# Kernel optimization log

Measured on AMD Instinct MI355X. Metric: run time of the kernel, lower is better.

The kernel has to match this reference:

```python
import jax, jax.numpy as jnp
import numpy as np

B, N, D_MODEL, LAP = 64, 64, 256, 16


def setup_inputs() -> dict:
    key = jax.random.key(0)
    ks = jax.random.split(key, 8)
    adj = jax.random.randint(ks[0], (B, N, N), 0, 2, dtype=jnp.int32)
    node_feats = jax.random.normal(ks[1], (B, N, D_MODEL), dtype=jnp.float32)
    eigvec = jax.random.normal(ks[2], (B, N, LAP), dtype=jnp.float32)
    W_lap = jax.random.normal(ks[3], (LAP, D_MODEL), dtype=jnp.float32) / np.sqrt(LAP)
    W_edge = jax.random.normal(ks[4], (1 + 2 * LAP, D_MODEL), dtype=jnp.float32) / np.sqrt(1 + 2 * LAP)
    b_edge = jax.random.normal(ks[5], (D_MODEL,), dtype=jnp.float32) * 0.02
    type_embed = jax.random.normal(ks[6], (2, D_MODEL), dtype=jnp.float32)
    graph_tok = jax.random.normal(ks[7], (1, 1, D_MODEL), dtype=jnp.float32)
    return {"adj": adj, "node_feats": node_feats, "eigvec": eigvec,
            "W_lap": W_lap, "W_edge": W_edge, "b_edge": b_edge,
            "type_embed": type_embed, "graph_tok": graph_tok}


def reference(adj, node_feats, eigvec, W_lap, W_edge, b_edge, type_embed, graph_tok):
    b, n, _ = adj.shape
    d = graph_tok.shape[-1]
    # node tokens: feats + LapPE projection
    node_tok = node_feats + jnp.einsum('bnl,ld->bnd', eigvec, W_lap)
    # upper-triangular candidate edges (fixed M = n(n-1)/2, jit-friendly)
    iu, ju = jnp.triu_indices(n, k=1)               # [M]
    valid = adj[:, iu, ju] > 0                       # [B, M]
    # stable compaction: valid edges first (matches torch per-graph extraction order)
    order = jnp.argsort(~valid, axis=1, stable=True) # [B, M]
    src = iu[order]                                  # [B, M]
    dst = ju[order]
    valid_sorted = jnp.take_along_axis(valid, order, axis=1)
    Pu = jnp.take_along_axis(eigvec, src[..., None], axis=1)  # [B, M, LAP]
    Pv = jnp.take_along_axis(eigvec, dst[..., None], axis=1)
    m = src.shape[1]
    edge_in = jnp.concatenate([jnp.ones((b, m, 1), eigvec.dtype), Pu, Pv], axis=-1)
    etok = jnp.einsum('bmf,fd->bmd', edge_in, W_edge) + b_edge + type_embed[1]
    etok = jnp.where(valid_sorted[..., None], etok, 0.0)      # zeros at padding
    pad_mask_edges = ~valid_sorted                             # True = padding
    gtok = jnp.broadcast_to(graph_tok, (b, 1, d))
    seq_embeds = jnp.concatenate([gtok, node_tok, etok], axis=1)  # [B, 1+n+M, d]
    pad_mask = jnp.concatenate([jnp.zeros((b, 1 + n), bool), pad_mask_edges], axis=1)
    return seq_embeds, pad_mask
```

## Files before the change

kernel.cpp:

```cpp
#include <hip/hip_runtime.h>

#define B_ 64
#define N_ 64
#define D_ 256
#define LAP_ 16
#define M_ 2016
#define TOK_ 2081

__global__ __launch_bounds__(256) void compact_kernel(const int* __restrict__ adj,
                                                      int* __restrict__ pack) {
    int b = blockIdx.x;
    int t = threadIdx.x;
    __shared__ int s[256];
    __shared__ int s_total;

    int ii[8], jj[8], vv[8];
    int c = 0;
#pragma unroll
    for (int k = 0; k < 8; k++) {
        int m = t * 8 + k;
        int valid = 0, i = 0, j = 0;
        if (m < M_) {
            float fm = (float)m;
            int gi = (int)((127.0f - sqrtf(127.0f * 127.0f - 8.0f * fm)) * 0.5f);
            if (gi < 0) gi = 0;
            if (gi > 62) gi = 62;
            while (gi > 0 && (127 * gi - gi * gi) / 2 > m) gi--;
            while (gi < 62 && (127 * (gi + 1) - (gi + 1) * (gi + 1)) / 2 <= m) gi++;
            i = gi;
            j = i + 1 + (m - (127 * i - i * i) / 2);
            valid = (adj[b * (N_ * N_) + i * N_ + j] > 0) ? 1 : 0;
        }
        ii[k] = i; jj[k] = j; vv[k] = valid;
        c += valid;
    }
    s[t] = c;
    __syncthreads();
    for (int off = 1; off < 256; off <<= 1) {
        int v = (t >= off) ? s[t - off] : 0;
        __syncthreads();
        s[t] += v;
        __syncthreads();
    }
    if (t == 255) s_total = s[255];
    __syncthreads();
    int total = s_total;
    int run = s[t] - c;
#pragma unroll
    for (int k = 0; k < 8; k++) {
        int m = t * 8 + k;
        if (m < M_) {
            int p;
            if (vv[k]) { p = run; run++; }
            else       { p = total + (m - run); }
            pack[b * M_ + p] = ii[k] | (jj[k] << 8) | (vv[k] << 16);
        }
    }
}

__global__ __launch_bounds__(256) void node_kernel(const float* __restrict__ node_feats,
                                                   const float* __restrict__ eigvec,
                                                   const float* __restrict__ W_lap,
                                                   const float* __restrict__ graph_tok,
                                                   float* __restrict__ out) {
    int b = blockIdx.x;
    int t = threadIdx.x;
    int n = blockIdx.y * 4 + (t >> 6);
    int lane = t & 63;
    const float* e = eigvec + (size_t)(b * N_ + n) * LAP_;
    float4 acc = ((const float4*)(node_feats + ((size_t)b * N_ + n) * D_))[lane];
#pragma unroll
    for (int l = 0; l < LAP_; l++) {
        float el = e[l];
        float4 w = ((const float4*)(W_lap + l * D_))[lane];
        acc.x += el * w.x; acc.y += el * w.y; acc.z += el * w.z; acc.w += el * w.w;
    }
    ((float4*)(out + (size_t)b * TOK_ * D_ + (size_t)(1 + n) * D_))[lane] = acc;

    if (blockIdx.y == 0) {
        out[(size_t)b * TOK_ * D_ + t] = graph_tok[t];
        float* mask = out + (size_t)B_ * TOK_ * D_;
        if (t < 1 + N_) mask[b * TOK_ + t] = 0.0f;
    }
}

__global__ __launch_bounds__(256) void edge_kernel(const float* __restrict__ eigvec,
                                                   const float* __restrict__ W_edge,
                                                   const float* __restrict__ b_edge,
                                                   const float* __restrict__ type_embed,
                                                   const int* __restrict__ pack,
                                                   float* __restrict__ out) {
    __shared__ float sEig[N_ * LAP_];

    int b = blockIdx.x;
    int t = threadIdx.x;
    int wave = t >> 6, lane = t & 63;

    ((float4*)sEig)[t] = ((const float4*)(eigvec + (size_t)b * N_ * LAP_))[t];

    float4 base = ((const float4*)W_edge)[lane];
    {
        float4 bb = ((const float4*)b_edge)[lane];
        float4 te = ((const float4*)(type_embed + D_))[lane];
        base.x += bb.x + te.x; base.y += bb.y + te.y;
        base.z += bb.z + te.z; base.w += bb.w + te.w;
    }
    float4 w1[LAP_], w2[LAP_];
#pragma unroll
    for (int l = 0; l < LAP_; l++) {
        w1[l] = ((const float4*)(W_edge + (1 + l) * D_))[lane];
        w2[l] = ((const float4*)(W_edge + (1 + LAP_ + l) * D_))[lane];
    }
    __syncthreads();

    float* maskb = out + (size_t)B_ * TOK_ * D_ + (size_t)b * TOK_ + 1 + N_;
    float* outb = out + (size_t)b * TOK_ * D_ + (size_t)(1 + N_) * D_;

#pragma unroll
    for (int k = 0; k < 8; k++) {
        int p = blockIdx.y * 32 + wave * 8 + k;
        int pk = pack[b * M_ + p];
        float4 acc = make_float4(0.f, 0.f, 0.f, 0.f);
        int valid = (pk >> 16) & 1;
        if (valid) {
            int si = pk & 0xff, di = (pk >> 8) & 0xff;
            const float4* eu4 = (const float4*)(sEig + si * LAP_);
            const float4* ev4 = (const float4*)(sEig + di * LAP_);
            float4 eu[4], ev[4];
#pragma unroll
            for (int q = 0; q < 4; q++) { eu[q] = eu4[q]; ev[q] = ev4[q]; }
            acc = base;
            const float* euf = (const float*)eu;
            const float* evf = (const float*)ev;
#pragma unroll
            for (int l = 0; l < LAP_; l++) {
                float pu = euf[l], pv = evf[l];
                acc.x += pu * w1[l].x + pv * w2[l].x;
                acc.y += pu * w1[l].y + pv * w2[l].y;
                acc.z += pu * w1[l].z + pv * w2[l].z;
                acc.w += pu * w1[l].w + pv * w2[l].w;
            }
        }
        ((float4*)(outb + (size_t)p * D_))[lane] = acc;
        if (lane == 0) maskb[p] = valid ? 0.0f : 1.0f;
    }
}

extern "C" void kernel_launch(void* const* d_in, const int* in_sizes, int n_in,
                              void* d_out, int out_size, void* d_ws, size_t ws_size,
                              hipStream_t stream) {
    const int*   adj        = (const int*)d_in[0];
    const float* node_feats = (const float*)d_in[1];
    const float* eigvec     = (const float*)d_in[2];
    const float* W_lap      = (const float*)d_in[3];
    const float* W_edge     = (const float*)d_in[4];
    const float* b_edge     = (const float*)d_in[5];
    const float* type_embed = (const float*)d_in[6];
    const float* graph_tok  = (const float*)d_in[7];
    float* out = (float*)d_out;
    int* pack = (int*)d_ws;

    compact_kernel<<<dim3(B_), dim3(256), 0, stream>>>(adj, pack);
    node_kernel<<<dim3(B_, 16), dim3(256), 0, stream>>>(node_feats, eigvec, W_lap,
                                                        graph_tok, out);
    edge_kernel<<<dim3(B_, 63), dim3(256), 0, stream>>>(eigvec, W_edge, b_edge,
                                                        type_embed, pack, out);
}
```

Measured before the change: 179.5 us.

## Fuse node and edge kernels, enlarge per-block edge work, use nontemporal stores

```diff
diff --git a/kernel.cpp b/kernel.cpp
--- a/kernel.cpp
+++ b/kernel.cpp
@@ -6,6 +6,13 @@
 #define LAP_ 16
 #define M_ 2016
 #define TOK_ 2081
+
+typedef float f32x4 __attribute__((ext_vector_type(4)));
+
+__device__ __forceinline__ void nt_store4(float* p, float4 v) {
+    f32x4 vv = {v.x, v.y, v.z, v.w};
+    __builtin_nontemporal_store(vv, (f32x4*)p);
+}
 
 __global__ __launch_bounds__(256) void compact_kernel(const int* __restrict__ adj,
                                                       int* __restrict__ pack) {
@@ -58,45 +65,44 @@
     }
 }
 
-__global__ __launch_bounds__(256) void node_kernel(const float* __restrict__ node_feats,
-                                                   const float* __restrict__ eigvec,
-                                                   const float* __restrict__ W_lap,
-                                                   const float* __restrict__ graph_tok,
-                                                   float* __restrict__ out) {
-    int b = blockIdx.x;
-    int t = threadIdx.x;
-    int n = blockIdx.y * 4 + (t >> 6);
-    int lane = t & 63;
-    const float* e = eigvec + (size_t)(b * N_ + n) * LAP_;
-    float4 acc = ((const float4*)(node_feats + ((size_t)b * N_ + n) * D_))[lane];
-#pragma unroll
-    for (int l = 0; l < LAP_; l++) {
-        float el = e[l];
-        float4 w = ((const float4*)(W_lap + l * D_))[lane];
-        acc.x += el * w.x; acc.y += el * w.y; acc.z += el * w.z; acc.w += el * w.w;
-    }
-    ((float4*)(out + (size_t)b * TOK_ * D_ + (size_t)(1 + n) * D_))[lane] = acc;
-
-    if (blockIdx.y == 0) {
-        out[(size_t)b * TOK_ * D_ + t] = graph_tok[t];
-        float* mask = out + (size_t)B_ * TOK_ * D_;
-        if (t < 1 + N_) mask[b * TOK_ + t] = 0.0f;
-    }
-}
-
-__global__ __launch_bounds__(256) void edge_kernel(const float* __restrict__ eigvec,
-                                                   const float* __restrict__ W_edge,
-                                                   const float* __restrict__ b_edge,
-                                                   const float* __restrict__ type_embed,
-                                                   const int* __restrict__ pack,
-                                                   float* __restrict__ out) {
+__global__ __launch_bounds__(256) void fused_kernel(const float* __restrict__ node_feats,
+                                                    const float* __restrict__ eigvec,
+                                                    const float* __restrict__ W_lap,
+                                                    const float* __restrict__ W_edge,
+                                                    const float* __restrict__ b_edge,
+                                                    const float* __restrict__ type_embed,
+                                                    const float* __restrict__ graph_tok,
+                                                    const int* __restrict__ pack,
+                                                    float* __restrict__ out) {
     __shared__ float sEig[N_ * LAP_];
-
     int b = blockIdx.x;
     int t = threadIdx.x;
     int wave = t >> 6, lane = t & 63;
 
     ((float4*)sEig)[t] = ((const float4*)(eigvec + (size_t)b * N_ * LAP_))[t];
+    __syncthreads();
+
+    if (blockIdx.y == 21) {
+        float* outb = out + (size_t)b * TOK_ * D_;
+#pragma unroll 1
+        for (int q = 0; q < 16; q++) {
+            int n = wave * 16 + q;
+            const float* e = sEig + n * LAP_;
+            float4 acc = ((const float4*)(node_feats + ((size_t)b * N_ + n) * D_))[lane];
+#pragma unroll
+            for (int l = 0; l < LAP_; l++) {
+                float el = e[l];
+                float4 w = ((const float4*)(W_lap + l * D_))[lane];
+                acc.x += el * w.x; acc.y += el * w.y;
+                acc.z += el * w.z; acc.w += el * w.w;
+            }
+            nt_store4(outb + (size_t)(1 + n) * D_ + lane * 4, acc);
+        }
+        outb[t] = graph_tok[t];
+        float* mask = out + (size_t)B_ * TOK_ * D_;
+        if (t < 1 + N_) mask[b * TOK_ + t] = 0.0f;
+        return;
+    }
 
     float4 base = ((const float4*)W_edge)[lane];
     {
@@ -111,37 +117,32 @@
         w1[l] = ((const float4*)(W_edge + (1 + l) * D_))[lane];
         w2[l] = ((const float4*)(W_edge + (1 + LAP_ + l) * D_))[lane];
     }
-    __syncthreads();
 
     float* maskb = out + (size_t)B_ * TOK_ * D_ + (size_t)b * TOK_ + 1 + N_;
     float* outb = out + (size_t)b * TOK_ * D_ + (size_t)(1 + N_) * D_;
+    int p0 = blockIdx.y * 96 + wave * 24;
 
-#pragma unroll
-    for (int k = 0; k < 8; k++) {
-        int p = blockIdx.y * 32 + wave * 8 + k;
+#pragma unroll 1
+    for (int k = 0; k < 24; k++) {
+        int p = p0 + k;
         int pk = pack[b * M_ + p];
+        int valid = (pk >> 16) & 1;
         float4 acc = make_float4(0.f, 0.f, 0.f, 0.f);
-        int valid = (pk >> 16) & 1;
         if (valid) {
             int si = pk & 0xff, di = (pk >> 8) & 0xff;
-            const float4* eu4 = (const float4*)(sEig + si * LAP_);
-            const float4* ev4 = (const float4*)(sEig + di * LAP_);
-            float4 eu[4], ev[4];
-#pragma unroll
-            for (int q = 0; q < 4; q++) { eu[q] = eu4[q]; ev[q] = ev4[q]; }
+            const float* eu = sEig + si * LAP_;
+            const float* ev = sEig + di * LAP_;
             acc = base;
-            const float* euf = (const float*)eu;
-            const float* evf = (const float*)ev;
 #pragma unroll
             for (int l = 0; l < LAP_; l++) {
-                float pu = euf[l], pv = evf[l];
+                float pu = eu[l], pv = ev[l];
                 acc.x += pu * w1[l].x + pv * w2[l].x;
                 acc.y += pu * w1[l].y + pv * w2[l].y;
                 acc.z += pu * w1[l].z + pv * w2[l].z;
                 acc.w += pu * w1[l].w + pv * w2[l].w;
             }
         }
-        ((float4*)(outb + (size_t)p * D_))[lane] = acc;
+        nt_store4(outb + (size_t)p * D_ + lane * 4, acc);
         if (lane == 0) maskb[p] = valid ? 0.0f : 1.0f;
     }
 }
@@ -161,8 +162,7 @@
     int* pack = (int*)d_ws;
 
     compact_kernel<<<dim3(B_), dim3(256), 0, stream>>>(adj, pack);
-    node_kernel<<<dim3(B_, 16), dim3(256), 0, stream>>>(node_feats, eigvec, W_lap,
-                                                        graph_tok, out);
-    edge_kernel<<<dim3(B_, 63), dim3(256), 0, stream>>>(eigvec, W_edge, b_edge,
-                                                        type_embed, pack, out);
+    fused_kernel<<<dim3(B_, 22), dim3(256), 0, stream>>>(node_feats, eigvec, W_lap,
+                                                         W_edge, b_edge, type_embed,
+                                                         graph_tok, pack, out);
 }
```

Result: slower. 191.0 us (+6.4%).
